# Kernel tuning notes

Measured on AMD Instinct MI355X. Metric: run time of the kernel, lower is better.

## Reference

```python
import jax, jax.numpy as jnp
import numpy as np

N_NODES = 50000
N_EDGES = 800000
D_FEAT = 64
N_CLASSES = 40


def setup_inputs() -> dict:
    key = jax.random.key(0)
    ks = jax.random.split(key, 8)
    x = jax.random.normal(ks[0], (N_NODES, D_FEAT), dtype=jnp.float32)
    edge_index = jax.random.randint(ks[1], (2, N_EDGES), 0, N_NODES, dtype=jnp.int64)
    # GCNConv weights (glorot-ish scale) and post-aggregation biases
    s1 = 1.0 / np.sqrt(D_FEAT)
    W1 = jax.random.normal(ks[2], (D_FEAT, D_FEAT), dtype=jnp.float32) * s1
    b1 = jnp.zeros((D_FEAT,), dtype=jnp.float32)
    W2 = jax.random.normal(ks[3], (D_FEAT, D_FEAT), dtype=jnp.float32) * s1
    b2 = jnp.zeros((D_FEAT,), dtype=jnp.float32)
    W3 = jax.random.normal(ks[4], (D_FEAT, N_CLASSES), dtype=jnp.float32) * s1
    b3 = jnp.zeros((N_CLASSES,), dtype=jnp.float32)
    return {"x": x, "edge_index": edge_index, "W1": W1, "b1": b1,
            "W2": W2, "b2": b2, "W3": W3, "b3": b3}


def _gcn_layer(x, src, dst, norm, W, b, n_nodes):
    # dense transform then normalized neighbor aggregation (PyG GCNConv)
    h = x @ W                                   # [N, out]
    msgs = h[src] * norm[:, None]               # gather over edges [E+N, out]
    agg = jax.ops.segment_sum(msgs, dst, num_segments=n_nodes)
    return agg + b


def reference(x, edge_index, W1, b1, W2, b2, W3, b3):
    n = x.shape[0]
    loops = jnp.arange(n, dtype=edge_index.dtype)
    src = jnp.concatenate([edge_index[0], loops])   # add self-loops
    dst = jnp.concatenate([edge_index[1], loops])
    # symmetric normalization: deg over targets incl. self-loops
    deg = jax.ops.segment_sum(jnp.ones_like(dst, dtype=x.dtype), dst, num_segments=n)
    dinv = jnp.where(deg > 0, jax.lax.rsqrt(deg), 0.0)
    norm = dinv[src] * dinv[dst]                    # [E+N]
    for W, b in ((W1, b1), (W2, b2), (W3, b3)):
        x = jax.nn.relu(_gcn_layer(x, src, dst, norm, W, b, n))
        # dropout treated as identity (deterministic eval reference)
    return jax.nn.log_softmax(x, axis=-1)
```

## Files before the change

kernel.cpp:

```cpp
#include <hip/hip_runtime.h>
#include <math.h>


#define DF 64
#define TB 256
#define NPART 8

typedef __attribute__((ext_vector_type(8))) short bf16x8;
typedef __attribute__((ext_vector_type(4))) float f32x4;

__device__ __forceinline__ unsigned short f2bf(float f) {
    union { float f; unsigned u; } c; c.f = f;
    unsigned u = c.u;
    return (unsigned short)((u + 0x7fffu + ((u >> 16) & 1u)) >> 16);
}
__device__ __forceinline__ float bf2f(unsigned short h) {
    union { unsigned u; float f; } c; c.u = ((unsigned)h) << 16;
    return c.f;
}
__device__ __forceinline__ void acc_bf16x8(uint4 v, float* a) {
    a[0] += bf2f((unsigned short)(v.x & 0xffffu));
    a[1] += bf2f((unsigned short)(v.x >> 16));
    a[2] += bf2f((unsigned short)(v.y & 0xffffu));
    a[3] += bf2f((unsigned short)(v.y >> 16));
    a[4] += bf2f((unsigned short)(v.z & 0xffffu));
    a[5] += bf2f((unsigned short)(v.z >> 16));
    a[6] += bf2f((unsigned short)(v.w & 0xffffu));
    a[7] += bf2f((unsigned short)(v.w >> 16));
}
__device__ __forceinline__ void acc_bf16x4(uint2 v, float* a) {
    a[0] += bf2f((unsigned short)(v.x & 0xffffu));
    a[1] += bf2f((unsigned short)(v.x >> 16));
    a[2] += bf2f((unsigned short)(v.y & 0xffffu));
    a[3] += bf2f((unsigned short)(v.y >> 16));
}

__global__ void zero_int_kernel(int* __restrict__ p, int n) {
    int i = blockIdx.x * blockDim.x + threadIdx.x;
    if (i < n) p[i] = 0;
}

__global__ void count_deg_part_kernel(const int* __restrict__ dst, int* __restrict__ deg,
                                      int e, int psize) {
    const int p   = blockIdx.x & (NPART - 1);
    const int sl  = blockIdx.x / NPART;
    const int nsl = gridDim.x / NPART;
    const int lo = p * psize, hi = lo + psize;
    for (int i = sl * TB + threadIdx.x; i < e; i += nsl * TB) {
        int d = dst[i];
        if (d >= lo && d < hi) atomicAdd(&deg[d], 1);
    }
}

__global__ void scan_block_kernel(const int* __restrict__ deg, int* __restrict__ ex,
                                  int* __restrict__ bsum, float* __restrict__ dinv, int n) {
    __shared__ int s[TB];
    const int t = threadIdx.x;
    const int i = blockIdx.x * TB + t;
    int v = (i < n) ? deg[i] : 0;
    if (i < n) dinv[i] = rsqrtf((float)(v + 1));
    s[t] = v; __syncthreads();
#pragma unroll
    for (int o = 1; o < TB; o <<= 1) {
        int u = (t >= o) ? s[t - o] : 0;
        __syncthreads();
        s[t] += u;
        __syncthreads();
    }
    if (i < n) ex[i] = s[t] - v;
    if (t == TB - 1) bsum[blockIdx.x] = s[TB - 1];
}

__global__ void add_offsets_kernel(int* __restrict__ ex, const int* __restrict__ bsum,
                                   int* __restrict__ cursor, int n, int nb) {
    __shared__ int s[TB];
    const int t = threadIdx.x;
    int v = (t < nb) ? bsum[t] : 0;
    s[t] = v; __syncthreads();
#pragma unroll
    for (int o = 1; o < TB; o <<= 1) {
        int u = (t >= o) ? s[t - o] : 0;
        __syncthreads();
        s[t] += u;
        __syncthreads();
    }
    const int boff = (blockIdx.x > 0) ? s[blockIdx.x - 1] : 0;
    const int i = blockIdx.x * TB + t;
    if (i < n) {
        int r = ex[i] + boff;
        ex[i] = r;
        cursor[i] = r;
    }
}

__global__ void fill_csr_part_kernel(const int* __restrict__ src, const int* __restrict__ dst,
                                     int* __restrict__ cursor,
                                     unsigned short* __restrict__ cidx, int e, int psize) {
    const int p   = blockIdx.x & (NPART - 1);
    const int sl  = blockIdx.x / NPART;
    const int nsl = gridDim.x / NPART;
    const int lo = p * psize, hi = lo + psize;
    for (int i = sl * TB + threadIdx.x; i < e; i += nsl * TB) {
        int d = dst[i];
        if (d >= lo && d < hi) {
            int pos = atomicAdd(&cursor[d], 1);
            cidx[pos] = (unsigned short)src[i];
        }
    }
}

__global__ __launch_bounds__(256) void gemm_mfma_kernel(
        const float* __restrict__ X, const float* __restrict__ W,
        const float* __restrict__ dinv, unsigned short* __restrict__ G, int M) {
    const int lane = threadIdx.x & 63;
    const int wid  = threadIdx.x >> 6;
    const int t    = blockIdx.x * 4 + wid;
    const int nt   = (M + 15) >> 4;
    if (t >= nt) return;
    const int n = lane & 15;
    const int g = lane >> 4;

    bf16x8 bf[4][2];
#pragma unroll
    for (int ct = 0; ct < 4; ++ct) {
        const int c = ct * 16 + n;
#pragma unroll
        for (int ks = 0; ks < 2; ++ks)
#pragma unroll
            for (int j = 0; j < 8; ++j)
                bf[ct][ks][j] = (short)f2bf(W[(ks * 32 + g * 8 + j) * 64 + c]);
    }

    const int row_a = t * 16 + n;
    const int ra = (row_a < M) ? row_a : (M - 1);
    bf16x8 af[2];
#pragma unroll
    for (int ks = 0; ks < 2; ++ks) {
        float4 p0 = *(const float4*)(X + (size_t)ra * 64 + ks * 32 + g * 8);
        float4 p1 = *(const float4*)(X + (size_t)ra * 64 + ks * 32 + g * 8 + 4);
        af[ks][0] = (short)f2bf(p0.x); af[ks][1] = (short)f2bf(p0.y);
        af[ks][2] = (short)f2bf(p0.z); af[ks][3] = (short)f2bf(p0.w);
        af[ks][4] = (short)f2bf(p1.x); af[ks][5] = (short)f2bf(p1.y);
        af[ks][6] = (short)f2bf(p1.z); af[ks][7] = (short)f2bf(p1.w);
    }

    const int rbase = t * 16 + g * 4;
    float di[4];
#pragma unroll
    for (int r = 0; r < 4; ++r) {
        int rr = rbase + r;
        di[r] = dinv[(rr < M) ? rr : (M - 1)];
    }

#pragma unroll
    for (int ct = 0; ct < 4; ++ct) {
        f32x4 acc = {0.f, 0.f, 0.f, 0.f};
        acc = __builtin_amdgcn_mfma_f32_16x16x32_bf16(af[0], bf[ct][0], acc, 0, 0, 0);
        acc = __builtin_amdgcn_mfma_f32_16x16x32_bf16(af[1], bf[ct][1], acc, 0, 0, 0);
        const int col = ct * 16 + n;
#pragma unroll
        for (int r = 0; r < 4; ++r) {
            const int row = rbase + r;
            if (row < M)
                G[(size_t)row * 64 + col] = f2bf(acc[r] * di[r]);
        }
    }
}

template <int NCO>
__global__ __launch_bounds__(256) void aggmm_kernel(
        const unsigned short* __restrict__ G,
        const int* __restrict__ rowptr, const int* __restrict__ deg,
        const unsigned short* __restrict__ cidx,
        const float* __restrict__ dinv, const float* __restrict__ b,
        const float* __restrict__ Wn,
        unsigned short* __restrict__ Gout, int M) {
    __shared__ unsigned short Ys[16][72];
    __shared__ float ds[16];
    const int tid  = threadIdx.x;
    const int lane = tid & 63;
    const int wid  = tid >> 6;
    const int base = blockIdx.x * 16;
    const int grp = lane >> 3;
    const int sub = lane & 7;
    const int n16 = lane & 15;
    const int g16 = lane >> 4;

    const bool wactive = (wid * 16 < NCO);
    bf16x8 bf[2];
    if (wactive) {
        const int c = wid * 16 + n16;
#pragma unroll
        for (int ks = 0; ks < 2; ++ks)
#pragma unroll
            for (int j = 0; j < 8; ++j) {
                const int k = ks * 32 + g16 * 8 + j;
                float w = (c < NCO) ? Wn[k * NCO + c] : 0.f;
                bf[ks][j] = (short)f2bf(w);
            }
    }

    for (int i = 0; i < 4; ++i) {
        const int nrow  = wid * 4 + i;
        const int node0 = base + nrow;
        const int node  = (node0 < M) ? node0 : (M - 1);
        const int start = rowptr[node];
        const int cnt   = deg[node];

        float a[8] = {0.f, 0.f, 0.f, 0.f, 0.f, 0.f, 0.f, 0.f};
        float c8[8] = {0.f, 0.f, 0.f, 0.f, 0.f, 0.f, 0.f, 0.f};
        for (int bs = 0; bs < cnt; bs += 64) {
            const int nthis = min(64, cnt - bs);
            int myidx = (lane < nthis) ? (int)cidx[start + bs + lane] : 0;
            int j = 0;
            for (; j + 16 <= nthis; j += 16) {
                int s0 = __shfl(myidx, j + grp, 64);
                int s1 = __shfl(myidx, j + 8 + grp, 64);
                uint4 v0 = *(const uint4*)(G + (size_t)s0 * 64 + sub * 8);
                uint4 v1 = *(const uint4*)(G + (size_t)s1 * 64 + sub * 8);
                acc_bf16x8(v0, a);
                acc_bf16x8(v1, c8);
            }
            if (j + 8 <= nthis) {
                int s0 = __shfl(myidx, j + grp, 64);
                uint4 v0 = *(const uint4*)(G + (size_t)s0 * 64 + sub * 8);
                acc_bf16x8(v0, a);
                j += 8;
            }
            const int rem = nthis - j;
            if (grp < rem) {
                int s0 = __shfl(myidx, j + grp, 64);
                uint4 v0 = *(const uint4*)(G + (size_t)s0 * 64 + sub * 8);
                acc_bf16x8(v0, c8);
            }
        }
#pragma unroll
        for (int k = 0; k < 8; ++k) a[k] += c8[k];
#pragma unroll
        for (int k = 0; k < 8; ++k) {
            a[k] += __shfl_xor(a[k], 8, 64);
            a[k] += __shfl_xor(a[k], 16, 64);
            a[k] += __shfl_xor(a[k], 32, 64);
        }
        if (grp == 0) {
            uint4 sv = *(const uint4*)(G + (size_t)node * 64 + sub * 8);
            float4 b0 = *(const float4*)(b + sub * 8);
            float4 b1 = *(const float4*)(b + sub * 8 + 4);
            const float di = dinv[node];
            float v[8];
            v[0] = fmaxf((a[0] + bf2f((unsigned short)(sv.x & 0xffffu))) * di + b0.x, 0.f);
            v[1] = fmaxf((a[1] + bf2f((unsigned short)(sv.x >> 16)))     * di + b0.y, 0.f);
            v[2] = fmaxf((a[2] + bf2f((unsigned short)(sv.y & 0xffffu))) * di + b0.z, 0.f);
            v[3] = fmaxf((a[3] + bf2f((unsigned short)(sv.y >> 16)))     * di + b0.w, 0.f);
            v[4] = fmaxf((a[4] + bf2f((unsigned short)(sv.z & 0xffffu))) * di + b1.x, 0.f);
            v[5] = fmaxf((a[5] + bf2f((unsigned short)(sv.z >> 16)))     * di + b1.y, 0.f);
            v[6] = fmaxf((a[6] + bf2f((unsigned short)(sv.w & 0xffffu))) * di + b1.z, 0.f);
            v[7] = fmaxf((a[7] + bf2f((unsigned short)(sv.w >> 16)))     * di + b1.w, 0.f);
            uint4 o;
            o.x = (unsigned)f2bf(v[0]) | ((unsigned)f2bf(v[1]) << 16);
            o.y = (unsigned)f2bf(v[2]) | ((unsigned)f2bf(v[3]) << 16);
            o.z = (unsigned)f2bf(v[4]) | ((unsigned)f2bf(v[5]) << 16);
            o.w = (unsigned)f2bf(v[6]) | ((unsigned)f2bf(v[7]) << 16);
            *((uint4*)&Ys[nrow][sub * 8]) = o;
            if (sub == 0) ds[nrow] = di;
        }
    }
    __syncthreads();

    if (!wactive) return;
    bf16x8 af[2];
#pragma unroll
    for (int ks = 0; ks < 2; ++ks)
        af[ks] = *(const bf16x8*)&Ys[n16][ks * 32 + g16 * 8];
    f32x4 acc = {0.f, 0.f, 0.f, 0.f};
    acc = __builtin_amdgcn_mfma_f32_16x16x32_bf16(af[0], bf[0], acc, 0, 0, 0);
    acc = __builtin_amdgcn_mfma_f32_16x16x32_bf16(af[1], bf[1], acc, 0, 0, 0);
    const int col = wid * 16 + n16;
#pragma unroll
    for (int r = 0; r < 4; ++r) {
        const int row = base + g16 * 4 + r;
        if (row < M && col < NCO)
            Gout[(size_t)row * NCO + col] = f2bf(acc[r] * ds[g16 * 4 + r]);
    }
}

__global__ void agg40_lsm_kernel(const unsigned short* __restrict__ G,
                                 const int* __restrict__ rowptr, const int* __restrict__ deg,
                                 const unsigned short* __restrict__ cidx,
                                 const float* __restrict__ dinv, const float* __restrict__ b,
                                 float* __restrict__ Y, int M) {
    constexpr int NC = 40;
    constexpr int NQ = 10;
    const int lane = threadIdx.x & 63;
    const int node = blockIdx.x * 4 + (threadIdx.x >> 6);
    if (node >= M) return;
    const int grp = lane >> 4;
    const int sub = lane & 15;
    const bool act = (sub < NQ);
    const int start = rowptr[node];
    const int cnt = deg[node];

    float a[4] = {0.f, 0.f, 0.f, 0.f};
    float c[4] = {0.f, 0.f, 0.f, 0.f};

    for (int base = 0; base < cnt; base += 64) {
        const int nthis = min(64, cnt - base);
        int myidx = (lane < nthis) ? (int)cidx[start + base + lane] : 0;
        int j = 0;
        for (; j + 8 <= nthis; j += 8) {
            int s0 = __shfl(myidx, j + grp, 64);
            int s1 = __shfl(myidx, j + 4 + grp, 64);
            if (act) {
                uint2 v0 = *(const uint2*)(G + (size_t)s0 * NC + sub * 4);
                uint2 v1 = *(const uint2*)(G + (size_t)s1 * NC + sub * 4);
                acc_bf16x4(v0, a);
                acc_bf16x4(v1, c);
            }
        }
        if (j + 4 <= nthis) {
            int s0 = __shfl(myidx, j + grp, 64);
            if (act) {
                uint2 v0 = *(const uint2*)(G + (size_t)s0 * NC + sub * 4);
                acc_bf16x4(v0, a);
            }
            j += 4;
        }
        const int rem = nthis - j;
        if (grp < rem) {
            int s0 = __shfl(myidx, j + grp, 64);
            if (act) {
                uint2 v0 = *(const uint2*)(G + (size_t)s0 * NC + sub * 4);
                acc_bf16x4(v0, c);
            }
        }
    }
#pragma unroll
    for (int k = 0; k < 4; ++k) a[k] += c[k];
#pragma unroll
    for (int k = 0; k < 4; ++k) {
        a[k] += __shfl_xor(a[k], 16, 64);
        a[k] += __shfl_xor(a[k], 32, 64);
    }
    float v[4];
    {
        float self[4] = {0.f, 0.f, 0.f, 0.f};
        float4 bb = make_float4(0.f, 0.f, 0.f, 0.f);
        if (act) {
            uint2 sv = *(const uint2*)(G + (size_t)node * NC + sub * 4);
            self[0] = bf2f((unsigned short)(sv.x & 0xffffu));
            self[1] = bf2f((unsigned short)(sv.x >> 16));
            self[2] = bf2f((unsigned short)(sv.y & 0xffffu));
            self[3] = bf2f((unsigned short)(sv.y >> 16));
            bb = *(const float4*)(b + sub * 4);
        }
        const float di = dinv[node];
        v[0] = fmaxf((a[0] + self[0]) * di + bb.x, 0.f);
        v[1] = fmaxf((a[1] + self[1]) * di + bb.y, 0.f);
        v[2] = fmaxf((a[2] + self[2]) * di + bb.z, 0.f);
        v[3] = fmaxf((a[3] + self[3]) * di + bb.w, 0.f);
    }
    float m = act ? fmaxf(fmaxf(v[0], v[1]), fmaxf(v[2], v[3])) : -INFINITY;
#pragma unroll
    for (int o = 1; o < 16; o <<= 1) m = fmaxf(m, __shfl_xor(m, o, 64));
    float es = act ? (expf(v[0] - m) + expf(v[1] - m) + expf(v[2] - m) + expf(v[3] - m)) : 0.f;
#pragma unroll
    for (int o = 1; o < 16; o <<= 1) es += __shfl_xor(es, o, 64);
    const float ls = logf(es);
    if (act && grp == 0) {
        *((float4*)(Y + (size_t)node * NC + sub * 4)) =
            make_float4(v[0] - m - ls, v[1] - m - ls, v[2] - m - ls, v[3] - m - ls);
    }
}

extern "C" void kernel_launch(void* const* d_in, const int* in_sizes, int n_in,
                              void* d_out, int out_size, void* d_ws, size_t ws_size,
                              hipStream_t stream) {
    const float* x  = (const float*)d_in[0];
    const int*   ei = (const int*)d_in[1];
    const float* W1 = (const float*)d_in[2];
    const float* b1 = (const float*)d_in[3];
    const float* W2 = (const float*)d_in[4];
    const float* b2 = (const float*)d_in[5];
    const float* W3 = (const float*)d_in[6];
    const float* b3 = (const float*)d_in[7];
    float* out = (float*)d_out;

    const int M  = in_sizes[0] / DF;
    const int E  = in_sizes[1] / 2;
    (void)ws_size; (void)n_in; (void)out_size;

    const int* src = ei;
    const int* dst = ei + E;

    const size_t Ma = ((size_t)M + 63) & ~63ull;
    const size_t Ea = ((size_t)E + 63) & ~63ull;

    int* deg    = (int*)d_ws;
    int* rowptr = deg + Ma;
    int* cursor = rowptr + Ma;
    int* bsum   = cursor + Ma;
    unsigned short* cidx = (unsigned short*)(bsum + 256);
    float* dinv = (float*)(cidx + Ea);
    unsigned short* G0 = (unsigned short*)(dinv + Ma);
    unsigned short* G1 = G0 + Ma * DF;

    const int gN = (M + TB - 1) / TB;
    const int nb = gN;
    const int psize = (M + NPART - 1) / NPART;
    const int partGrd = NPART * 96;

    zero_int_kernel<<<gN, TB, 0, stream>>>(deg, M);
    count_deg_part_kernel<<<partGrd, TB, 0, stream>>>(dst, deg, E, psize);
    scan_block_kernel<<<nb, TB, 0, stream>>>(deg, rowptr, bsum, dinv, M);
    add_offsets_kernel<<<nb, TB, 0, stream>>>(rowptr, bsum, cursor, M, nb);
    fill_csr_part_kernel<<<partGrd, TB, 0, stream>>>(src, dst, cursor, cidx, E, psize);

    const int nt      = (M + 15) / 16;
    const int gemmGrd = (nt + 3) / 4;
    const int fusGrd  = nt;
    const int aggGrd  = (M + 3) / 4;

    gemm_mfma_kernel<<<gemmGrd, TB, 0, stream>>>(x, W1, dinv, G0, M);
    aggmm_kernel<64><<<fusGrd, TB, 0, stream>>>(G0, rowptr, deg, cidx, dinv, b1, W2, G1, M);
    aggmm_kernel<40><<<fusGrd, TB, 0, stream>>>(G1, rowptr, deg, cidx, dinv, b2, W3, G0, M);
    agg40_lsm_kernel<<<aggGrd, TB, 0, stream>>>(G0, rowptr, deg, cidx, dinv, b3, out, M);
}
```

Measured before the change: 194.6 us.

## Split 64-wide bf16 feature tables into two 32-column planes for gathers

The hidden-feature matrices are stored as two separate 32-column bf16 planes instead of one 64-column row-major table. The fused aggregate+GEMM kernel gathers neighbours in two passes, one per half, each with 8-byte loads. This shrinks the random-gather working set per pass so it is more likely to stay in L2. In exchange, the neighbour index reads, shuffles and reductions are done twice, and each gather is narrower.

```diff
diff --git a/kernel.cpp b/kernel.cpp
--- a/kernel.cpp
+++ b/kernel.cpp
@@ -17,16 +17,6 @@
 __device__ __forceinline__ float bf2f(unsigned short h) {
     union { unsigned u; float f; } c; c.u = ((unsigned)h) << 16;
     return c.f;
-}
-__device__ __forceinline__ void acc_bf16x8(uint4 v, float* a) {
-    a[0] += bf2f((unsigned short)(v.x & 0xffffu));
-    a[1] += bf2f((unsigned short)(v.x >> 16));
-    a[2] += bf2f((unsigned short)(v.y & 0xffffu));
-    a[3] += bf2f((unsigned short)(v.y >> 16));
-    a[4] += bf2f((unsigned short)(v.z & 0xffffu));
-    a[5] += bf2f((unsigned short)(v.z >> 16));
-    a[6] += bf2f((unsigned short)(v.w & 0xffffu));
-    a[7] += bf2f((unsigned short)(v.w >> 16));
 }
 __device__ __forceinline__ void acc_bf16x4(uint2 v, float* a) {
     a[0] += bf2f((unsigned short)(v.x & 0xffffu));
@@ -111,7 +101,8 @@
 
 __global__ __launch_bounds__(256) void gemm_mfma_kernel(
         const float* __restrict__ X, const float* __restrict__ W,
-        const float* __restrict__ dinv, unsigned short* __restrict__ G, int M) {
+        const float* __restrict__ dinv,
+        unsigned short* __restrict__ Glo, unsigned short* __restrict__ Ghi, int M) {
     const int lane = threadIdx.x & 63;
     const int wid  = threadIdx.x >> 6;
     const int t    = blockIdx.x * 4 + wid;
@@ -157,32 +148,33 @@
         f32x4 acc = {0.f, 0.f, 0.f, 0.f};
         acc = __builtin_amdgcn_mfma_f32_16x16x32_bf16(af[0], bf[ct][0], acc, 0, 0, 0);
         acc = __builtin_amdgcn_mfma_f32_16x16x32_bf16(af[1], bf[ct][1], acc, 0, 0, 0);
-        const int col = ct * 16 + n;
+        unsigned short* plane = (ct < 2) ? Glo : Ghi;
+        const int c32 = (ct & 1) * 16 + n;
 #pragma unroll
         for (int r = 0; r < 4; ++r) {
             const int row = rbase + r;
             if (row < M)
-                G[(size_t)row * 64 + col] = f2bf(acc[r] * di[r]);
+                plane[(size_t)row * 32 + c32] = f2bf(acc[r] * di[r]);
         }
     }
 }
 
 template <int NCO>
 __global__ __launch_bounds__(256) void aggmm_kernel(
-        const unsigned short* __restrict__ G,
+        const unsigned short* __restrict__ Glo, const unsigned short* __restrict__ Ghi,
         const int* __restrict__ rowptr, const int* __restrict__ deg,
         const unsigned short* __restrict__ cidx,
         const float* __restrict__ dinv, const float* __restrict__ b,
         const float* __restrict__ Wn,
-        unsigned short* __restrict__ Gout, int M) {
+        unsigned short* __restrict__ Olo, unsigned short* __restrict__ Ohi, int M) {
     __shared__ unsigned short Ys[16][72];
     __shared__ float ds[16];
     const int tid  = threadIdx.x;
     const int lane = tid & 63;
     const int wid  = tid >> 6;
     const int base = blockIdx.x * 16;
-    const int grp = lane >> 3;
-    const int sub = lane & 7;
+    const int grp8 = lane >> 3;
+    const int sub8 = lane & 7;
     const int n16 = lane & 15;
     const int g16 = lane >> 4;
 
@@ -200,69 +192,65 @@
             }
     }
 
-    for (int i = 0; i < 4; ++i) {
-        const int nrow  = wid * 4 + i;
-        const int node0 = base + nrow;
-        const int node  = (node0 < M) ? node0 : (M - 1);
-        const int start = rowptr[node];
-        const int cnt   = deg[node];
-
-        float a[8] = {0.f, 0.f, 0.f, 0.f, 0.f, 0.f, 0.f, 0.f};
-        float c8[8] = {0.f, 0.f, 0.f, 0.f, 0.f, 0.f, 0.f, 0.f};
-        for (int bs = 0; bs < cnt; bs += 64) {
-            const int nthis = min(64, cnt - bs);
-            int myidx = (lane < nthis) ? (int)cidx[start + bs + lane] : 0;
-            int j = 0;
-            for (; j + 16 <= nthis; j += 16) {
-                int s0 = __shfl(myidx, j + grp, 64);
-                int s1 = __shfl(myidx, j + 8 + grp, 64);
-                uint4 v0 = *(const uint4*)(G + (size_t)s0 * 64 + sub * 8);
-                uint4 v1 = *(const uint4*)(G + (size_t)s1 * 64 + sub * 8);
-                acc_bf16x8(v0, a);
-                acc_bf16x8(v1, c8);
-            }
-            if (j + 8 <= nthis) {
-                int s0 = __shfl(myidx, j + grp, 64);
-                uint4 v0 = *(const uint4*)(G + (size_t)s0 * 64 + sub * 8);
-                acc_bf16x8(v0, a);
-                j += 8;
-            }
-            const int rem = nthis - j;
-            if (grp < rem) {
-                int s0 = __shfl(myidx, j + grp, 64);
-                uint4 v0 = *(const uint4*)(G + (size_t)s0 * 64 + sub * 8);
-                acc_bf16x8(v0, c8);
-            }
-        }
-#pragma unroll
-        for (int k = 0; k < 8; ++k) a[k] += c8[k];
-#pragma unroll
-        for (int k = 0; k < 8; ++k) {
-            a[k] += __shfl_xor(a[k], 8, 64);
-            a[k] += __shfl_xor(a[k], 16, 64);
-            a[k] += __shfl_xor(a[k], 32, 64);
-        }
-        if (grp == 0) {
-            uint4 sv = *(const uint4*)(G + (size_t)node * 64 + sub * 8);
-            float4 b0 = *(const float4*)(b + sub * 8);
-            float4 b1 = *(const float4*)(b + sub * 8 + 4);
-            const float di = dinv[node];
-            float v[8];
-            v[0] = fmaxf((a[0] + bf2f((unsigned short)(sv.x & 0xffffu))) * di + b0.x, 0.f);
-            v[1] = fmaxf((a[1] + bf2f((unsigned short)(sv.x >> 16)))     * di + b0.y, 0.f);
-            v[2] = fmaxf((a[2] + bf2f((unsigned short)(sv.y & 0xffffu))) * di + b0.z, 0.f);
-            v[3] = fmaxf((a[3] + bf2f((unsigned short)(sv.y >> 16)))     * di + b0.w, 0.f);
-            v[4] = fmaxf((a[4] + bf2f((unsigned short)(sv.z & 0xffffu))) * di + b1.x, 0.f);
-            v[5] = fmaxf((a[5] + bf2f((unsigned short)(sv.z >> 16)))     * di + b1.y, 0.f);
-            v[6] = fmaxf((a[6] + bf2f((unsigned short)(sv.w & 0xffffu))) * di + b1.z, 0.f);
-            v[7] = fmaxf((a[7] + bf2f((unsigned short)(sv.w >> 16)))     * di + b1.w, 0.f);
-            uint4 o;
-            o.x = (unsigned)f2bf(v[0]) | ((unsigned)f2bf(v[1]) << 16);
-            o.y = (unsigned)f2bf(v[2]) | ((unsigned)f2bf(v[3]) << 16);
-            o.z = (unsigned)f2bf(v[4]) | ((unsigned)f2bf(v[5]) << 16);
-            o.w = (unsigned)f2bf(v[6]) | ((unsigned)f2bf(v[7]) << 16);
-            *((uint4*)&Ys[nrow][sub * 8]) = o;
-            if (sub == 0) ds[nrow] = di;
+#pragma unroll
+    for (int half = 0; half < 2; ++half) {
+        const unsigned short* Gh = half ? Ghi : Glo;
+        for (int i = 0; i < 4; ++i) {
+            const int nrow  = wid * 4 + i;
+            const int node0 = base + nrow;
+            const int node  = (node0 < M) ? node0 : (M - 1);
+            const int start = rowptr[node];
+            const int cnt   = deg[node];
+
+            float a[4] = {0.f, 0.f, 0.f, 0.f};
+            float c4[4] = {0.f, 0.f, 0.f, 0.f};
+            for (int bs = 0; bs < cnt; bs += 64) {
+                const int nthis = min(64, cnt - bs);
+                int myidx = (lane < nthis) ? (int)cidx[start + bs + lane] : 0;
+                int j = 0;
+                for (; j + 16 <= nthis; j += 16) {
+                    int s0 = __shfl(myidx, j + grp8, 64);
+                    int s1 = __shfl(myidx, j + 8 + grp8, 64);
+                    uint2 v0 = *(const uint2*)(Gh + (size_t)s0 * 32 + sub8 * 4);
+                    uint2 v1 = *(const uint2*)(Gh + (size_t)s1 * 32 + sub8 * 4);
+                    acc_bf16x4(v0, a);
+                    acc_bf16x4(v1, c4);
+                }
+                if (j + 8 <= nthis) {
+                    int s0 = __shfl(myidx, j + grp8, 64);
+                    uint2 v0 = *(const uint2*)(Gh + (size_t)s0 * 32 + sub8 * 4);
+                    acc_bf16x4(v0, a);
+                    j += 8;
+                }
+                const int rem = nthis - j;
+                if (grp8 < rem) {
+                    int s0 = __shfl(myidx, j + grp8, 64);
+                    uint2 v0 = *(const uint2*)(Gh + (size_t)s0 * 32 + sub8 * 4);
+                    acc_bf16x4(v0, c4);
+                }
+            }
+#pragma unroll
+            for (int k = 0; k < 4; ++k) a[k] += c4[k];
+#pragma unroll
+            for (int k = 0; k < 4; ++k) {
+                a[k] += __shfl_xor(a[k], 8, 64);
+                a[k] += __shfl_xor(a[k], 16, 64);
+                a[k] += __shfl_xor(a[k], 32, 64);
+            }
+            if (grp8 == 0) {
+                uint2 sv = *(const uint2*)(Gh + (size_t)node * 32 + sub8 * 4);
+                float4 bb = *(const float4*)(b + half * 32 + sub8 * 4);
+                const float di = dinv[node];
+                float v0 = fmaxf((a[0] + bf2f((unsigned short)(sv.x & 0xffffu))) * di + bb.x, 0.f);
+                float v1 = fmaxf((a[1] + bf2f((unsigned short)(sv.x >> 16)))     * di + bb.y, 0.f);
+                float v2 = fmaxf((a[2] + bf2f((unsigned short)(sv.y & 0xffffu))) * di + bb.z, 0.f);
+                float v3 = fmaxf((a[3] + bf2f((unsigned short)(sv.y >> 16)))     * di + bb.w, 0.f);
+                uint2 o;
+                o.x = (unsigned)f2bf(v0) | ((unsigned)f2bf(v1) << 16);
+                o.y = (unsigned)f2bf(v2) | ((unsigned)f2bf(v3) << 16);
+                *((uint2*)&Ys[nrow][half * 32 + sub8 * 4]) = o;
+                if (half == 0 && sub8 == 0) ds[nrow] = di;
+            }
         }
     }
     __syncthreads();
@@ -279,8 +267,15 @@
 #pragma unroll
     for (int r = 0; r < 4; ++r) {
         const int row = base + g16 * 4 + r;
-        if (row < M && col < NCO)
-            Gout[(size_t)row * NCO + col] = f2bf(acc[r] * ds[g16 * 4 + r]);
+        if (row < M && col < NCO) {
+            const unsigned short y = f2bf(acc[r] * ds[g16 * 4 + r]);
+            if (NCO == 64) {
+                unsigned short* plane = (wid < 2) ? Olo : Ohi;
+                plane[(size_t)row * 32 + (wid & 1) * 16 + n16] = y;
+            } else {
+                Olo[(size_t)row * NCO + col] = y;
+            }
+        }
     }
 }
 
@@ -401,8 +396,11 @@
     int* bsum   = cursor + Ma;
     unsigned short* cidx = (unsigned short*)(bsum + 256);
     float* dinv = (float*)(cidx + Ea);
-    unsigned short* G0 = (unsigned short*)(dinv + Ma);
-    unsigned short* G1 = G0 + Ma * DF;
+    unsigned short* G0lo = (unsigned short*)(dinv + Ma);
+    unsigned short* G0hi = G0lo + Ma * 32;
+    unsigned short* G1lo = G0hi + Ma * 32;
+    unsigned short* G1hi = G1lo + Ma * 32;
+    unsigned short* G3   = G0lo;
 
     const int gN = (M + TB - 1) / TB;
     const int nb = gN;
@@ -420,8 +418,10 @@
     const int fusGrd  = nt;
     const int aggGrd  = (M + 3) / 4;
 
-    gemm_mfma_kernel<<<gemmGrd, TB, 0, stream>>>(x, W1, dinv, G0, M);
-    aggmm_kernel<64><<<fusGrd, TB, 0, stream>>>(G0, rowptr, deg, cidx, dinv, b1, W2, G1, M);
-    aggmm_kernel<40><<<fusGrd, TB, 0, stream>>>(G1, rowptr, deg, cidx, dinv, b2, W3, G0, M);
-    agg40_lsm_kernel<<<aggGrd, TB, 0, stream>>>(G0, rowptr, deg, cidx, dinv, b3, out, M);
-}
+    gemm_mfma_kernel<<<gemmGrd, TB, 0, stream>>>(x, W1, dinv, G0lo, G0hi, M);
+    aggmm_kernel<64><<<fusGrd, TB, 0, stream>>>(G0lo, G0hi, rowptr, deg, cidx,
+                                                dinv, b1, W2, G1lo, G1hi, M);
+    aggmm_kernel<40><<<fusGrd, TB, 0, stream>>>(G1lo, G1hi, rowptr, deg, cidx,
+                                                dinv, b2, W3, G3, nullptr, M);
+    agg40_lsm_kernel<<<aggGrd, TB, 0, stream>>>(G3, rowptr, deg, cidx, dinv, b3, out, M);
+}
```

After: 229.2 us. 1.18x slower.
